# Kernel tuning notes

Measured on AMD Instinct MI355X. Metric: run time of the kernel, lower is better.

Reference implementation:

```python
import jax, jax.numpy as jnp
import numpy as np

DT = 0.1
EM_DX_DUMMY = 100.0  # dummy_value_set['em_delta_x']
EM_DV_DUMMY = 0.0    # dummy_value_set['em_delta_v']
ALPHA = 0.3          # keras LeakyReLU default
B, T, F = 32768, 50, 11
PROJ, U = 64, 128
MC = 3
IN_DIM = PROJ + U + 6 + MC  # 201


def setup_inputs() -> dict:
    key = jax.random.key(0)
    ks = jax.random.split(key, 16)
    def rn(k, shape, scale=0.05):
        return jax.random.normal(k, shape, dtype=jnp.float32) * scale
    return {
        'proj_latent': rn(ks[0], (B, PROJ), 1.0),
        'enc_h': rn(ks[1], (B, U), 1.0),
        'idm_s': jax.random.uniform(ks[2], (B, T, F), dtype=jnp.float32),
        'merger_cs': rn(ks[3], (B, T, MC), 1.0),
        'scaler_mean': rn(ks[4], (6,), 1.0),
        'scaler_var': jax.random.uniform(ks[5], (6,), dtype=jnp.float32) + 0.5,
        'W_lstm': rn(ks[6], (IN_DIM, 4 * U)),
        'U_lstm': rn(ks[7], (U, 4 * U)),
        'b_lstm': jnp.zeros((4 * U,), jnp.float32),
        'W1': rn(ks[8], (U, U)), 'b1': jnp.zeros((U,), jnp.float32),
        'W2': rn(ks[9], (U, U)), 'b2': jnp.zeros((U,), jnp.float32),
        'W3': rn(ks[10], (U, U)), 'b3': jnp.zeros((U,), jnp.float32),
        'Wa': rn(ks[11], (U, 1)), 'ba': jnp.zeros((1,), jnp.float32),
    }


def _lrelu(v):
    return jnp.where(v > 0, v, ALPHA * v)


def reference(proj_latent, enc_h, idm_s, merger_cs, scaler_mean, scaler_var,
              W_lstm, U_lstm, b_lstm, W1, b1, W2, b2, W3, b3, Wa, ba):
    b = idm_s.shape[0]
    u = W1.shape[0]
    inv_std = 1.0 / jnp.sqrt(scaler_var)

    def step(carry, xs):
        h, c, ego_v, ego_x, disp, prev_act = carry
        s, mc, t = xs  # s: [b,F], mc: [b,MC]
        first = (t == 0)
        f_veh_v = s[:, 1:2]
        m_veh_v = s[:, 2:3]
        f_glob_x = s[:, 4:5]
        m_glob_x = s[:, 5:6]
        m_exists = s[:, -1:]
        # physics update (skipped at step 0 where state is read from idm_s)
        new_v = jnp.where(first, s[:, 0:1], ego_v + prev_act * DT)
        delta = new_v * DT + 0.5 * prev_act * DT * DT
        new_x = jnp.where(first, s[:, 3:4], ego_x + delta)
        new_d = jnp.where(first, jnp.zeros_like(disp), disp + delta)
        ef_dx = f_glob_x - new_x
        em_dx = (m_glob_x - new_x) * m_exists + (1.0 - m_exists) * EM_DX_DUMMY
        ef_dv = new_v - f_veh_v
        em_dv = (new_v - m_veh_v) * m_exists + (1.0 - m_exists) * EM_DV_DUMMY
        env = jnp.concatenate([new_v, f_veh_v, ef_dv, ef_dx, em_dv, em_dx], axis=-1)
        env = (env - scaler_mean) * inv_std
        inp = jnp.concatenate([proj_latent, enc_h, env, mc], axis=-1)  # [b, 201]
        # keras LSTM cell: gate order i, f, g(candidate), o
        z = inp @ W_lstm + h @ U_lstm + b_lstm
        i = jax.nn.sigmoid(z[:, :u])
        f = jax.nn.sigmoid(z[:, u:2 * u])
        g = jnp.tanh(z[:, 2 * u:3 * u])
        o = jax.nn.sigmoid(z[:, 3 * u:])
        c2 = f * c + i * g
        h2 = o * jnp.tanh(c2)
        x1 = _lrelu(h2 @ W1 + b1)
        x2 = _lrelu(x1 @ W2 + b2)
        x3 = _lrelu(x2 @ W3 + b3)
        act = x3 @ Wa + ba  # [b, 1]
        return (h2, c2, new_v, new_x, new_d, act), (new_d, act)

    z1 = jnp.zeros((b, u), jnp.float32)
    one = jnp.zeros((b, 1), jnp.float32)
    carry0 = (z1, z1, one, one, one, one)
    xs = (jnp.swapaxes(idm_s, 0, 1), jnp.swapaxes(merger_cs, 0, 1),
          jnp.arange(idm_s.shape[1]))
    _, (disp_seq, act_seq) = jax.lax.scan(step, carry0, xs)
    # [T,b,1] -> [b,T,1]
    return jnp.swapaxes(disp_seq, 0, 1), jnp.swapaxes(act_seq, 0, 1)
```

## Files before the change

kernel.cpp:

```cpp
#include <hip/hip_runtime.h>

typedef unsigned short ushort_t;
typedef unsigned int uint_t;
typedef __bf16 v8bf __attribute__((ext_vector_type(8)));
typedef float v4f __attribute__((ext_vector_type(4)));

#define DTC 0.1f
#define NB 32768
#define NT 50

union U8 { v8bf v; ushort_t s[8]; };

__device__ __forceinline__ ushort_t f2bf(float f) {
  uint_t u = __float_as_uint(f);
  u += 0x7fffu + ((u >> 16) & 1u);
  return (ushort_t)(u >> 16);
}
__device__ __forceinline__ float bf2f(ushort_t s) {
  return __uint_as_float(((uint_t)s) << 16);
}
__device__ __forceinline__ float sigm(float x) {
  return __builtin_amdgcn_rcpf(1.f + __expf(-x));
}
__device__ __forceinline__ float tanhf_(float x) {
  return 1.f - 2.f * __builtin_amdgcn_rcpf(1.f + __expf(2.f * x));
}

__device__ __forceinline__ v8bf opaque(v8bf x) {
  union { v8bf v; uint_t u[4]; } t; t.v = x;
  asm volatile("" : "+v"(t.u[0]), "+v"(t.u[1]), "+v"(t.u[2]), "+v"(t.u[3]));
  return t.v;
}


__global__ __launch_bounds__(512) __attribute__((amdgpu_waves_per_eu(2, 2)))
void fsim_kernel(
    const float* __restrict__ proj, const float* __restrict__ ench,
    const float* __restrict__ idm,  const float* __restrict__ mcs,
    const float* __restrict__ smean,const float* __restrict__ svar,
    const float* __restrict__ Wl,   const float* __restrict__ Ul,
    const float* __restrict__ bl,   const float* __restrict__ W1,
    const float* __restrict__ b1,   const float* __restrict__ W2,
    const float* __restrict__ b2,   const float* __restrict__ W3,
    const float* __restrict__ b3,   const float* __restrict__ Wa,
    const float* __restrict__ ba,   float* __restrict__ out) {
  __shared__ __align__(16) short sh[81184];
  short* pe   = sh;
  short* h_s  = sh;
  short* xa_s = sh + 8704;
  short* xb_s = sh + 17408;
  short* ex_s = sh + 26112;
  float* sdf  = (float*)(sh + 28672);
  float* carr = (float*)(sh + 31232);
  float* wa_s = (float*)(sh + 31744);
  float* nrm  = (float*)(sh + 32000);
  float* part = (float*)(sh + 17408);
  short* w1_l = sh + 32032;
  short* w2_l = sh + 48416;
  short* w3_l = sh + 64800;

  const int tid  = threadIdx.x;
  const int wg   = blockIdx.x;
  const int w    = tid >> 6;
  const int l    = tid & 63;
  const int quad = l >> 4;
  const int c16  = l & 15;
  const int colz = w * 16 + c16;

  float* out_disp = out;
  float* out_act  = out + (size_t)NB * NT;

  const int eA = tid / 10, fA = tid - eA * 10;
  const float* pfpA; int pstA;
  if (fA < 7) { pfpA = idm + (size_t)(wg * 64 + eA) * 550 + ((fA == 6) ? 10 : fA); pstA = 11; }
  else        { pfpA = mcs + (size_t)(wg * 64 + eA) * 150 + (fA - 7);              pstA = 3;  }
  const int iB = tid + 512;
  const int eB = iB / 10, fB = iB - eB * 10;
  const float* pfpB; int pstB;
  if (fB < 7) { pfpB = idm + (size_t)(wg * 64 + eB) * 550 + ((fB == 6) ? 10 : fB); pstB = 11; }
  else        { pfpB = mcs + (size_t)(wg * 64 + eB) * 150 + (fB - 7);              pstB = 3;  }
  float pfA = pfpA[0];
  float pfB = (tid < 128) ? pfpB[0] : 0.f;

  v8bf Uf[4][4];
#pragma unroll
  for (int kc = 0; kc < 4; ++kc) {
#pragma unroll
    for (int g = 0; g < 4; ++g) {
      U8 u;
#pragma unroll
      for (int j = 0; j < 8; ++j)
        u.s[j] = f2bf(Ul[(kc * 32 + quad * 8 + j) * 512 + g * 128 + colz]);
      Uf[kc][g] = opaque(u.v);
    }
  }
  v8bf Ef[4];
#pragma unroll
  for (int g = 0; g < 4; ++g) {
    U8 u;
#pragma unroll
    for (int j = 0; j < 8; ++j) {
      int kk = quad * 8 + j;
      ushort_t val = 0;
      if (kk < 27) {
        int jj = kk % 9;
        float wv = Wl[(192 + jj) * 512 + g * 128 + colz];
        ushort_t hi = f2bf(wv);
        val = (kk < 9) ? hi : ((kk < 18) ? f2bf(wv - bf2f(hi)) : hi);
      }
      u.s[j] = val;
    }
    Ef[g] = opaque(u.v);
  }

#pragma unroll
  for (int kc = 0; kc < 4; ++kc) {
    U8 a, b, c;
#pragma unroll
    for (int j = 0; j < 8; ++j) {
      int row = kc * 32 + quad * 8 + j;
      a.s[j] = f2bf(W1[row * 128 + colz]);
      b.s[j] = f2bf(W2[row * 128 + colz]);
      c.s[j] = f2bf(W3[row * 128 + colz]);
    }
    *(v8bf*)(w1_l + (kc * 512 + tid) * 8) = a.v;
    *(v8bf*)(w2_l + (kc * 512 + tid) * 8) = b.v;
    *(v8bf*)(w3_l + (kc * 512 + tid) * 8) = c.v;
  }

  float bias1 = b1[colz], bias2 = b2[colz], bias3 = b3[colz];
  float ba_v  = ba[0];

  for (int i = tid; i < 2560; i += 512) ex_s[i] = 0;
  if (tid < 6) { nrm[tid] = smean[tid]; nrm[6 + tid] = 1.f / sqrtf(svar[tid]); }
  if (tid < 128) wa_s[tid] = Wa[tid];
  sdf[tid] = pfA;
  if (tid < 128) sdf[512 + tid] = pfB;

  for (int i = tid; i < 64 * 192; i += 512) {
    int e = i / 192, j = i - e * 192;
    float v = (j < 64) ? proj[(wg * 64 + e) * 64 + j]
                       : ench[(wg * 64 + e) * 128 + (j - 64)];
    pe[e * 200 + j] = (short)f2bf(v);
  }
  __syncthreads();

  uint_t base_pk[4][8];
#pragma unroll
  for (int mt = 0; mt < 4; ++mt) {
    v4f accz[4];
#pragma unroll
    for (int g = 0; g < 4; ++g) {
      float bz = bl[g * 128 + colz];
      accz[g] = (v4f){bz, bz, bz, bz};
    }
    for (int kc = 0; kc < 6; ++kc) {
      const v8bf a = *(const v8bf*)(pe + (mt * 16 + c16) * 200 + kc * 32 + quad * 8);
#pragma unroll
      for (int g = 0; g < 4; ++g) {
        U8 bu;
#pragma unroll
        for (int j = 0; j < 8; ++j)
          bu.s[j] = f2bf(Wl[(kc * 32 + quad * 8 + j) * 512 + g * 128 + colz]);
        accz[g] = __builtin_amdgcn_mfma_f32_16x16x32_bf16(a, bu.v, accz[g], 0, 0, 0);
      }
    }
#pragma unroll
    for (int g = 0; g < 4; ++g) {
      base_pk[mt][g * 2 + 0] = (uint_t)f2bf(accz[g][0]) | ((uint_t)f2bf(accz[g][1]) << 16);
      base_pk[mt][g * 2 + 1] = (uint_t)f2bf(accz[g][2]) | ((uint_t)f2bf(accz[g][3]) << 16);
    }
  }
  __syncthreads();

  for (int i = tid; i < 8704; i += 512) h_s[i] = 0;

  v4f c_st[4];
#pragma unroll
  for (int mt = 0; mt < 4; ++mt) c_st[mt] = (v4f){0.f, 0.f, 0.f, 0.f};

  for (int t = 0; t < NT; ++t) {
    if (t + 1 < NT) {
      pfA = pfpA[(size_t)(t + 1) * pstA];
      if (tid < 128) pfB = pfpB[(size_t)(t + 1) * pstB];
    }

    if (w == 0) {
      const int e  = l;
      const int ge = wg * 64 + e;
      const float* sp = sdf + (t & 1) * 640 + e * 10;
      float s0 = sp[0], s1 = sp[1], s2 = sp[2], s3 = sp[3];
      float s4 = sp[4], s5 = sp[5], s10 = sp[6];
      float mc0 = sp[7], mc1 = sp[8], mc2 = sp[9];
      float pa = 0.f, vv = 0.f, xx = 0.f, dd = 0.f;
      if (t != 0) { pa = carr[192 + e]; vv = carr[e]; xx = carr[64 + e]; dd = carr[128 + e]; }
      float new_v = (t == 0) ? s0 : vv + pa * DTC;
      float delta = new_v * DTC + 0.5f * pa * DTC * DTC;
      float new_x = (t == 0) ? s3 : xx + delta;
      float new_d = (t == 0) ? 0.f : dd + delta;
      float env[9];
      env[0] = new_v;
      env[1] = s1;
      env[2] = new_v - s1;
      env[3] = s4 - new_x;
      env[4] = (new_v - s2) * s10;
      env[5] = (s5 - new_x) * s10 + (1.f - s10) * 100.f;
#pragma unroll
      for (int j = 0; j < 6; ++j) env[j] = (env[j] - nrm[j]) * nrm[6 + j];
      env[6] = mc0; env[7] = mc1; env[8] = mc2;
#pragma unroll
      for (int j = 0; j < 9; ++j) {
        ushort_t hi = f2bf(env[j]);
        ushort_t lo = f2bf(env[j] - bf2f(hi));
        ex_s[e * 40 + j]      = (short)hi;
        ex_s[e * 40 + 9 + j]  = (short)hi;
        ex_s[e * 40 + 18 + j] = (short)lo;
      }
      carr[e] = new_v; carr[64 + e] = new_x; carr[128 + e] = new_d;
      out_disp[(size_t)ge * NT + t] = new_d;
    }
    __syncthreads();

    v4f h2v[4];
#pragma unroll
    for (int mt = 0; mt < 4; ++mt) {
      v4f acc[4];
#pragma unroll
      for (int g = 0; g < 4; ++g) {
        uint_t w0 = base_pk[mt][g * 2 + 0], w1 = base_pk[mt][g * 2 + 1];
        acc[g][0] = __uint_as_float(w0 << 16);
        acc[g][1] = __uint_as_float(w0 & 0xffff0000u);
        acc[g][2] = __uint_as_float(w1 << 16);
        acc[g][3] = __uint_as_float(w1 & 0xffff0000u);
      }
#pragma unroll
      for (int kc = 0; kc < 4; ++kc) {
        const v8bf a = *(const v8bf*)(h_s + (mt * 16 + c16) * 136 + kc * 32 + quad * 8);
#pragma unroll
        for (int g = 0; g < 4; ++g)
          acc[g] = __builtin_amdgcn_mfma_f32_16x16x32_bf16(a, Uf[kc][g], acc[g], 0, 0, 0);
      }
      {
        const v8bf ax = *(const v8bf*)(ex_s + (mt * 16 + c16) * 40 + quad * 8);
#pragma unroll
        for (int g = 0; g < 4; ++g)
          acc[g] = __builtin_amdgcn_mfma_f32_16x16x32_bf16(ax, Ef[g], acc[g], 0, 0, 0);
      }
      v4f cc = c_st[mt], h2;
#pragma unroll
      for (int r = 0; r < 4; ++r) {
        float ig = sigm(acc[0][r]);
        float fg = sigm(acc[1][r]);
        float gg = tanhf_(acc[2][r]);
        float og = sigm(acc[3][r]);
        float c2 = fg * cc[r] + ig * gg;
        cc[r] = c2;
        h2[r] = og * tanhf_(c2);
      }
      c_st[mt] = cc;
      h2v[mt]  = h2;
    }
    __syncthreads();
#pragma unroll
    for (int mt = 0; mt < 4; ++mt)
#pragma unroll
      for (int r = 0; r < 4; ++r)
        h_s[(mt * 16 + quad * 4 + r) * 136 + colz] = (short)f2bf(h2v[mt][r]);
    __syncthreads();

    auto mlp_layer = [&](const short* S, const short* WL, float bias, short* D) {
      v8bf Wf[4];
#pragma unroll
      for (int kc = 0; kc < 4; ++kc)
        Wf[kc] = *(const v8bf*)(WL + (kc * 512 + tid) * 8);
      v4f xs[4];
#pragma unroll
      for (int mt = 0; mt < 4; ++mt) {
        v4f acc = (v4f){bias, bias, bias, bias};
#pragma unroll
        for (int kc = 0; kc < 4; ++kc) {
          const v8bf a = *(const v8bf*)(S + (mt * 16 + c16) * 136 + kc * 32 + quad * 8);
          acc = __builtin_amdgcn_mfma_f32_16x16x32_bf16(a, Wf[kc], acc, 0, 0, 0);
        }
#pragma unroll
        for (int r = 0; r < 4; ++r) { float v = acc[r]; acc[r] = (v > 0.f) ? v : 0.3f * v; }
        xs[mt] = acc;
      }
#pragma unroll
      for (int mt = 0; mt < 4; ++mt)
#pragma unroll
        for (int r = 0; r < 4; ++r)
          D[(mt * 16 + quad * 4 + r) * 136 + colz] = (short)f2bf(xs[mt][r]);
    };
    mlp_layer(h_s, w1_l, bias1, xa_s);
    __syncthreads();
    mlp_layer(xa_s, w2_l, bias2, xb_s);
    __syncthreads();
    mlp_layer(xb_s, w3_l, bias3, xa_s);
    __syncthreads();

    {
      int e = tid >> 3, p = tid & 7;
      float s = 0.f;
#pragma unroll
      for (int i = 0; i < 16; ++i) {
        int u = p * 16 + i;
        s += bf2f((ushort_t)xa_s[e * 136 + u]) * wa_s[u];
      }
      part[e * 8 + p] = s;
    }
    if (t + 1 < NT) {
      sdf[((t + 1) & 1) * 640 + tid] = pfA;
      if (tid < 128) sdf[((t + 1) & 1) * 640 + 512 + tid] = pfB;
    }
    __syncthreads();
    if (tid < 64) {
      float a = ba_v;
#pragma unroll
      for (int p = 0; p < 8; ++p) a += part[tid * 8 + p];
      carr[192 + tid] = a;
      out_act[(size_t)(wg * 64 + tid) * NT + t] = a;
    }
  }
}

extern "C" void kernel_launch(void* const* d_in, const int* in_sizes, int n_in,
                              void* d_out, int out_size, void* d_ws, size_t ws_size,
                              hipStream_t stream) {
  (void)in_sizes; (void)n_in; (void)out_size; (void)d_ws; (void)ws_size;
  fsim_kernel<<<dim3(512), dim3(512), 0, stream>>>(
      (const float*)d_in[0],  (const float*)d_in[1],  (const float*)d_in[2],
      (const float*)d_in[3],  (const float*)d_in[4],  (const float*)d_in[5],
      (const float*)d_in[6],  (const float*)d_in[7],  (const float*)d_in[8],
      (const float*)d_in[9],  (const float*)d_in[10], (const float*)d_in[11],
      (const float*)d_in[12], (const float*)d_in[13], (const float*)d_in[14],
      (const float*)d_in[15], (const float*)d_in[16], (float*)d_out);
}
```

Baseline: 967.2 us.

## Prepack weights to bf16 in a separate kernel and stream them from global memory

Adds a small pre-kernel that converts and packs the LSTM recurrent, env and MLP weights into MFMA fragment layout in the workspace each call. The main kernel stops holding U/E fragments in registers and stops staging MLP weights in LDS, instead reading them from global memory (expected to hit L1/L2) inside every time step. This frees registers and cuts LDS from about 162KB to 64KB, and the waves-per-EU hint rises from 2 to 4 to raise occupancy. The cost is many repeated global loads per step on the critical recurrent path, plus an extra launch.

New measurement: 2.834 ms. 2.93x slower.

```diff
diff --git a/kernel.cpp b/kernel.cpp
--- a/kernel.cpp
+++ b/kernel.cpp
@@ -26,25 +26,59 @@
   return 1.f - 2.f * __builtin_amdgcn_rcpf(1.f + __expf(2.f * x));
 }
 
-__device__ __forceinline__ v8bf opaque(v8bf x) {
-  union { v8bf v; uint_t u[4]; } t; t.v = x;
-  asm volatile("" : "+v"(t.u[0]), "+v"(t.u[1]), "+v"(t.u[2]), "+v"(t.u[3]));
-  return t.v;
-}
-
-
-__global__ __launch_bounds__(512) __attribute__((amdgpu_waves_per_eu(2, 2)))
+
+__global__ __launch_bounds__(512)
+void pack_kernel(const float* __restrict__ Ul, const float* __restrict__ Wl,
+                 const float* __restrict__ W1, const float* __restrict__ W2,
+                 const float* __restrict__ W3, ushort_t* __restrict__ ws) {
+  const int tid  = threadIdx.x;
+  const int b    = blockIdx.x;
+  const int l    = tid & 63;
+  const int wv   = tid >> 6;
+  const int quad = l >> 4;
+  const int c16  = l & 15;
+  const int colz = wv * 16 + c16;
+  U8 u;
+  if (b < 16) {
+    int kc = b >> 2, g = b & 3;
+#pragma unroll
+    for (int j = 0; j < 8; ++j)
+      u.s[j] = f2bf(Ul[(kc * 32 + quad * 8 + j) * 512 + g * 128 + colz]);
+  } else if (b < 20) {
+    int g = b - 16;
+#pragma unroll
+    for (int j = 0; j < 8; ++j) {
+      int kk = quad * 8 + j;
+      ushort_t val = 0;
+      if (kk < 27) {
+        int jj = kk % 9;
+        float wvv = Wl[(192 + jj) * 512 + g * 128 + colz];
+        ushort_t hi = f2bf(wvv);
+        val = (kk < 9) ? hi : ((kk < 18) ? f2bf(wvv - bf2f(hi)) : hi);
+      }
+      u.s[j] = val;
+    }
+  } else {
+    int m = (b - 20) >> 2, kc = (b - 20) & 3;
+    const float* Wp = (m == 0) ? W1 : ((m == 1) ? W2 : W3);
+#pragma unroll
+    for (int j = 0; j < 8; ++j)
+      u.s[j] = f2bf(Wp[(kc * 32 + quad * 8 + j) * 128 + colz]);
+  }
+  *(v8bf*)(ws + (size_t)b * 4096 + (size_t)tid * 8) = u.v;
+}
+
+__global__ __launch_bounds__(512) __attribute__((amdgpu_waves_per_eu(4, 4)))
 void fsim_kernel(
     const float* __restrict__ proj, const float* __restrict__ ench,
     const float* __restrict__ idm,  const float* __restrict__ mcs,
     const float* __restrict__ smean,const float* __restrict__ svar,
-    const float* __restrict__ Wl,   const float* __restrict__ Ul,
-    const float* __restrict__ bl,   const float* __restrict__ W1,
-    const float* __restrict__ b1,   const float* __restrict__ W2,
-    const float* __restrict__ b2,   const float* __restrict__ W3,
+    const float* __restrict__ Wl,   const float* __restrict__ bl,
+    const float* __restrict__ b1,   const float* __restrict__ b2,
     const float* __restrict__ b3,   const float* __restrict__ Wa,
-    const float* __restrict__ ba,   float* __restrict__ out) {
-  __shared__ __align__(16) short sh[81184];
+    const float* __restrict__ ba,   const ushort_t* __restrict__ ws,
+    float* __restrict__ out) {
+  __shared__ __align__(16) short sh[32032];
   short* pe   = sh;
   short* h_s  = sh;
   short* xa_s = sh + 8704;
@@ -55,9 +89,6 @@
   float* wa_s = (float*)(sh + 31744);
   float* nrm  = (float*)(sh + 32000);
   float* part = (float*)(sh + 17408);
-  short* w1_l = sh + 32032;
-  short* w2_l = sh + 48416;
-  short* w3_l = sh + 64800;
 
   const int tid  = threadIdx.x;
   const int wg   = blockIdx.x;
@@ -69,6 +100,7 @@
 
   float* out_disp = out;
   float* out_act  = out + (size_t)NB * NT;
+  const ushort_t* wsb = ws + (size_t)tid * 8;
 
   const int eA = tid / 10, fA = tid - eA * 10;
   const float* pfpA; int pstA;
@@ -81,52 +113,6 @@
   else        { pfpB = mcs + (size_t)(wg * 64 + eB) * 150 + (fB - 7);              pstB = 3;  }
   float pfA = pfpA[0];
   float pfB = (tid < 128) ? pfpB[0] : 0.f;
-
-  v8bf Uf[4][4];
-#pragma unroll
-  for (int kc = 0; kc < 4; ++kc) {
-#pragma unroll
-    for (int g = 0; g < 4; ++g) {
-      U8 u;
-#pragma unroll
-      for (int j = 0; j < 8; ++j)
-        u.s[j] = f2bf(Ul[(kc * 32 + quad * 8 + j) * 512 + g * 128 + colz]);
-      Uf[kc][g] = opaque(u.v);
-    }
-  }
-  v8bf Ef[4];
-#pragma unroll
-  for (int g = 0; g < 4; ++g) {
-    U8 u;
-#pragma unroll
-    for (int j = 0; j < 8; ++j) {
-      int kk = quad * 8 + j;
-      ushort_t val = 0;
-      if (kk < 27) {
-        int jj = kk % 9;
-        float wv = Wl[(192 + jj) * 512 + g * 128 + colz];
-        ushort_t hi = f2bf(wv);
-        val = (kk < 9) ? hi : ((kk < 18) ? f2bf(wv - bf2f(hi)) : hi);
-      }
-      u.s[j] = val;
-    }
-    Ef[g] = opaque(u.v);
-  }
-
-#pragma unroll
-  for (int kc = 0; kc < 4; ++kc) {
-    U8 a, b, c;
-#pragma unroll
-    for (int j = 0; j < 8; ++j) {
-      int row = kc * 32 + quad * 8 + j;
-      a.s[j] = f2bf(W1[row * 128 + colz]);
-      b.s[j] = f2bf(W2[row * 128 + colz]);
-      c.s[j] = f2bf(W3[row * 128 + colz]);
-    }
-    *(v8bf*)(w1_l + (kc * 512 + tid) * 8) = a.v;
-    *(v8bf*)(w2_l + (kc * 512 + tid) * 8) = b.v;
-    *(v8bf*)(w3_l + (kc * 512 + tid) * 8) = c.v;
-  }
 
   float bias1 = b1[colz], bias2 = b2[colz], bias3 = b3[colz];
   float ba_v  = ba[0];
@@ -237,14 +223,18 @@
       for (int kc = 0; kc < 4; ++kc) {
         const v8bf a = *(const v8bf*)(h_s + (mt * 16 + c16) * 136 + kc * 32 + quad * 8);
 #pragma unroll
-        for (int g = 0; g < 4; ++g)
-          acc[g] = __builtin_amdgcn_mfma_f32_16x16x32_bf16(a, Uf[kc][g], acc[g], 0, 0, 0);
+        for (int g = 0; g < 4; ++g) {
+          const v8bf uf = *(const v8bf*)(wsb + (size_t)(kc * 4 + g) * 4096);
+          acc[g] = __builtin_amdgcn_mfma_f32_16x16x32_bf16(a, uf, acc[g], 0, 0, 0);
+        }
       }
       {
         const v8bf ax = *(const v8bf*)(ex_s + (mt * 16 + c16) * 40 + quad * 8);
 #pragma unroll
-        for (int g = 0; g < 4; ++g)
-          acc[g] = __builtin_amdgcn_mfma_f32_16x16x32_bf16(ax, Ef[g], acc[g], 0, 0, 0);
+        for (int g = 0; g < 4; ++g) {
+          const v8bf ef = *(const v8bf*)(wsb + (size_t)(16 + g) * 4096);
+          acc[g] = __builtin_amdgcn_mfma_f32_16x16x32_bf16(ax, ef, acc[g], 0, 0, 0);
+        }
       }
       v4f cc = c_st[mt], h2;
 #pragma unroll
@@ -268,11 +258,11 @@
         h_s[(mt * 16 + quad * 4 + r) * 136 + colz] = (short)f2bf(h2v[mt][r]);
     __syncthreads();
 
-    auto mlp_layer = [&](const short* S, const short* WL, float bias, short* D) {
+    auto mlp_layer = [&](const short* S, const ushort_t* WF, float bias, short* D) {
       v8bf Wf[4];
 #pragma unroll
       for (int kc = 0; kc < 4; ++kc)
-        Wf[kc] = *(const v8bf*)(WL + (kc * 512 + tid) * 8);
+        Wf[kc] = *(const v8bf*)(WF + (size_t)kc * 4096);
       v4f xs[4];
 #pragma unroll
       for (int mt = 0; mt < 4; ++mt) {
@@ -292,11 +282,11 @@
         for (int r = 0; r < 4; ++r)
           D[(mt * 16 + quad * 4 + r) * 136 + colz] = (short)f2bf(xs[mt][r]);
     };
-    mlp_layer(h_s, w1_l, bias1, xa_s);
-    __syncthreads();
-    mlp_layer(xa_s, w2_l, bias2, xb_s);
-    __syncthreads();
-    mlp_layer(xb_s, w3_l, bias3, xa_s);
+    mlp_layer(h_s, wsb + (size_t)20 * 4096, bias1, xa_s);
+    __syncthreads();
+    mlp_layer(xa_s, wsb + (size_t)24 * 4096, bias2, xb_s);
+    __syncthreads();
+    mlp_layer(xb_s, wsb + (size_t)28 * 4096, bias3, xa_s);
     __syncthreads();
 
     {
@@ -327,12 +317,14 @@
 extern "C" void kernel_launch(void* const* d_in, const int* in_sizes, int n_in,
                               void* d_out, int out_size, void* d_ws, size_t ws_size,
                               hipStream_t stream) {
-  (void)in_sizes; (void)n_in; (void)out_size; (void)d_ws; (void)ws_size;
+  (void)in_sizes; (void)n_in; (void)out_size; (void)ws_size;
+  pack_kernel<<<dim3(32), dim3(512), 0, stream>>>(
+      (const float*)d_in[7],  (const float*)d_in[6],  (const float*)d_in[9],
+      (const float*)d_in[11], (const float*)d_in[13], (ushort_t*)d_ws);
   fsim_kernel<<<dim3(512), dim3(512), 0, stream>>>(
       (const float*)d_in[0],  (const float*)d_in[1],  (const float*)d_in[2],
       (const float*)d_in[3],  (const float*)d_in[4],  (const float*)d_in[5],
-      (const float*)d_in[6],  (const float*)d_in[7],  (const float*)d_in[8],
-      (const float*)d_in[9],  (const float*)d_in[10], (const float*)d_in[11],
-      (const float*)d_in[12], (const float*)d_in[13], (const float*)d_in[14],
-      (const float*)d_in[15], (const float*)d_in[16], (float*)d_out);
-}
+      (const float*)d_in[6],  (const float*)d_in[8],  (const float*)d_in[10],
+      (const float*)d_in[12], (const float*)d_in[14], (const float*)d_in[15],
+      (const float*)d_in[16], (const ushort_t*)d_ws,  (float*)d_out);
+}
```

## Double-buffer LSTM hidden state, keep MLP weights in registers, shuffle-reduce the action head

Applied to the files above, without the earlier changes.

Ping-pongs the hidden-state LDS buffer so the new h is written right after the gate math, with no extra barrier. The MLP weights now live in registers, and three quarters of the recurrent U matrix moves to LDS to free VGPRs. The output projection is reduced with lane shuffles, and the environment update is spread across all waves. Together these remove several __syncthreads per timestep and LDS round-trips, at the cost of extra LDS reads of U every step and higher register pressure.

Result: slower. 1.017 ms (+5.2%).

```diff
diff --git a/kernel.cpp b/kernel.cpp
--- a/kernel.cpp
+++ b/kernel.cpp
@@ -46,18 +46,15 @@
     const float* __restrict__ ba,   float* __restrict__ out) {
   __shared__ __align__(16) short sh[81184];
   short* pe   = sh;
-  short* h_s  = sh;
-  short* xa_s = sh + 8704;
-  short* xb_s = sh + 17408;
+  short* hA   = sh;
+  short* hB   = sh + 8704;
+  short* xa_s = sh + 17408;
   short* ex_s = sh + 26112;
   float* sdf  = (float*)(sh + 28672);
   float* carr = (float*)(sh + 31232);
   float* wa_s = (float*)(sh + 31744);
   float* nrm  = (float*)(sh + 32000);
-  float* part = (float*)(sh + 17408);
-  short* w1_l = sh + 32032;
-  short* w2_l = sh + 48416;
-  short* w3_l = sh + 64800;
+  short* u_lds= sh + 32032;
 
   const int tid  = threadIdx.x;
   const int wg   = blockIdx.x;
@@ -82,17 +79,25 @@
   float pfA = pfpA[0];
   float pfB = (tid < 128) ? pfpB[0] : 0.f;
 
-  v8bf Uf[4][4];
-#pragma unroll
-  for (int kc = 0; kc < 4; ++kc) {
+#pragma unroll
+  for (int kc = 0; kc < 3; ++kc) {
 #pragma unroll
     for (int g = 0; g < 4; ++g) {
       U8 u;
 #pragma unroll
       for (int j = 0; j < 8; ++j)
         u.s[j] = f2bf(Ul[(kc * 32 + quad * 8 + j) * 512 + g * 128 + colz]);
-      Uf[kc][g] = opaque(u.v);
-    }
+      *(v8bf*)(u_lds + ((kc * 4 + g) * 512 + tid) * 8) = u.v;
+    }
+  }
+  v8bf Uf3[4];
+#pragma unroll
+  for (int g = 0; g < 4; ++g) {
+    U8 u;
+#pragma unroll
+    for (int j = 0; j < 8; ++j)
+      u.s[j] = f2bf(Ul[(96 + quad * 8 + j) * 512 + g * 128 + colz]);
+    Uf3[g] = opaque(u.v);
   }
   v8bf Ef[4];
 #pragma unroll
@@ -112,7 +117,7 @@
     }
     Ef[g] = opaque(u.v);
   }
-
+  v8bf W1f[4], W2f[4], W3f[4];
 #pragma unroll
   for (int kc = 0; kc < 4; ++kc) {
     U8 a, b, c;
@@ -123,11 +128,8 @@
       b.s[j] = f2bf(W2[row * 128 + colz]);
       c.s[j] = f2bf(W3[row * 128 + colz]);
     }
-    *(v8bf*)(w1_l + (kc * 512 + tid) * 8) = a.v;
-    *(v8bf*)(w2_l + (kc * 512 + tid) * 8) = b.v;
-    *(v8bf*)(w3_l + (kc * 512 + tid) * 8) = c.v;
-  }
-
+    W1f[kc] = opaque(a.v); W2f[kc] = opaque(b.v); W3f[kc] = opaque(c.v);
+  }
   float bias1 = b1[colz], bias2 = b2[colz], bias3 = b3[colz];
   float ba_v  = ba[0];
 
@@ -173,20 +175,23 @@
   }
   __syncthreads();
 
-  for (int i = tid; i < 8704; i += 512) h_s[i] = 0;
+  for (int i = tid; i < 8704; i += 512) hA[i] = 0;
 
   v4f c_st[4];
 #pragma unroll
   for (int mt = 0; mt < 4; ++mt) c_st[mt] = (v4f){0.f, 0.f, 0.f, 0.f};
 
   for (int t = 0; t < NT; ++t) {
+    short* rd = (t & 1) ? hB : hA;
+    short* wr = (t & 1) ? hA : hB;
+
     if (t + 1 < NT) {
       pfA = pfpA[(size_t)(t + 1) * pstA];
       if (tid < 128) pfB = pfpB[(size_t)(t + 1) * pstB];
     }
 
-    if (w == 0) {
-      const int e  = l;
+    if ((l & 7) == 0) {
+      const int e  = w * 8 + (l >> 3);
       const int ge = wg * 64 + e;
       const float* sp = sdf + (t & 1) * 640 + e * 10;
       float s0 = sp[0], s1 = sp[1], s2 = sp[2], s3 = sp[3];
@@ -221,58 +226,66 @@
     }
     __syncthreads();
 
-    v4f h2v[4];
-#pragma unroll
-    for (int mt = 0; mt < 4; ++mt) {
-      v4f acc[4];
-#pragma unroll
-      for (int g = 0; g < 4; ++g) {
-        uint_t w0 = base_pk[mt][g * 2 + 0], w1 = base_pk[mt][g * 2 + 1];
-        acc[g][0] = __uint_as_float(w0 << 16);
-        acc[g][1] = __uint_as_float(w0 & 0xffff0000u);
-        acc[g][2] = __uint_as_float(w1 << 16);
-        acc[g][3] = __uint_as_float(w1 & 0xffff0000u);
+#pragma unroll
+    for (int half = 0; half < 2; ++half) {
+      v4f acc[2][4];
+#pragma unroll
+      for (int m2 = 0; m2 < 2; ++m2) {
+        int mt = half * 2 + m2;
+#pragma unroll
+        for (int g = 0; g < 4; ++g) {
+          uint_t w0 = base_pk[mt][g * 2 + 0], w1 = base_pk[mt][g * 2 + 1];
+          acc[m2][g][0] = __uint_as_float(w0 << 16);
+          acc[m2][g][1] = __uint_as_float(w0 & 0xffff0000u);
+          acc[m2][g][2] = __uint_as_float(w1 << 16);
+          acc[m2][g][3] = __uint_as_float(w1 & 0xffff0000u);
+        }
+      }
+      {
+        const v8bf ax0 = *(const v8bf*)(ex_s + ((half * 2 + 0) * 16 + c16) * 40 + quad * 8);
+        const v8bf ax1 = *(const v8bf*)(ex_s + ((half * 2 + 1) * 16 + c16) * 40 + quad * 8);
+#pragma unroll
+        for (int g = 0; g < 4; ++g) {
+          acc[0][g] = __builtin_amdgcn_mfma_f32_16x16x32_bf16(ax0, Ef[g], acc[0][g], 0, 0, 0);
+          acc[1][g] = __builtin_amdgcn_mfma_f32_16x16x32_bf16(ax1, Ef[g], acc[1][g], 0, 0, 0);
+        }
       }
 #pragma unroll
       for (int kc = 0; kc < 4; ++kc) {
-        const v8bf a = *(const v8bf*)(h_s + (mt * 16 + c16) * 136 + kc * 32 + quad * 8);
-#pragma unroll
-        for (int g = 0; g < 4; ++g)
-          acc[g] = __builtin_amdgcn_mfma_f32_16x16x32_bf16(a, Uf[kc][g], acc[g], 0, 0, 0);
-      }
-      {
-        const v8bf ax = *(const v8bf*)(ex_s + (mt * 16 + c16) * 40 + quad * 8);
-#pragma unroll
-        for (int g = 0; g < 4; ++g)
-          acc[g] = __builtin_amdgcn_mfma_f32_16x16x32_bf16(ax, Ef[g], acc[g], 0, 0, 0);
-      }
-      v4f cc = c_st[mt], h2;
-#pragma unroll
-      for (int r = 0; r < 4; ++r) {
-        float ig = sigm(acc[0][r]);
-        float fg = sigm(acc[1][r]);
-        float gg = tanhf_(acc[2][r]);
-        float og = sigm(acc[3][r]);
-        float c2 = fg * cc[r] + ig * gg;
-        cc[r] = c2;
-        h2[r] = og * tanhf_(c2);
-      }
-      c_st[mt] = cc;
-      h2v[mt]  = h2;
-    }
-    __syncthreads();
-#pragma unroll
-    for (int mt = 0; mt < 4; ++mt)
-#pragma unroll
-      for (int r = 0; r < 4; ++r)
-        h_s[(mt * 16 + quad * 4 + r) * 136 + colz] = (short)f2bf(h2v[mt][r]);
-    __syncthreads();
-
-    auto mlp_layer = [&](const short* S, const short* WL, float bias, short* D) {
-      v8bf Wf[4];
-#pragma unroll
-      for (int kc = 0; kc < 4; ++kc)
-        Wf[kc] = *(const v8bf*)(WL + (kc * 512 + tid) * 8);
+        const v8bf a0 = *(const v8bf*)(rd + ((half * 2 + 0) * 16 + c16) * 136 + kc * 32 + quad * 8);
+        const v8bf a1 = *(const v8bf*)(rd + ((half * 2 + 1) * 16 + c16) * 136 + kc * 32 + quad * 8);
+#pragma unroll
+        for (int g = 0; g < 4; ++g) {
+          v8bf uf;
+          if (kc < 3) uf = *(const v8bf*)(u_lds + ((kc * 4 + g) * 512 + tid) * 8);
+          else        uf = Uf3[g];
+          acc[0][g] = __builtin_amdgcn_mfma_f32_16x16x32_bf16(a0, uf, acc[0][g], 0, 0, 0);
+          acc[1][g] = __builtin_amdgcn_mfma_f32_16x16x32_bf16(a1, uf, acc[1][g], 0, 0, 0);
+        }
+      }
+#pragma unroll
+      for (int m2 = 0; m2 < 2; ++m2) {
+        int mt = half * 2 + m2;
+        v4f cc = c_st[mt], h2;
+#pragma unroll
+        for (int r = 0; r < 4; ++r) {
+          float ig = sigm(acc[m2][0][r]);
+          float fg = sigm(acc[m2][1][r]);
+          float gg = tanhf_(acc[m2][2][r]);
+          float og = sigm(acc[m2][3][r]);
+          float c2 = fg * cc[r] + ig * gg;
+          cc[r] = c2;
+          h2[r] = og * tanhf_(c2);
+        }
+        c_st[mt] = cc;
+#pragma unroll
+        for (int r = 0; r < 4; ++r)
+          wr[(mt * 16 + quad * 4 + r) * 136 + colz] = (short)f2bf(h2[r]);
+      }
+    }
+    __syncthreads();
+
+    auto mlp_layer = [&](const short* S, const v8bf* Wf, float bias, short* D) {
       v4f xs[4];
 #pragma unroll
       for (int mt = 0; mt < 4; ++mt) {
@@ -292,34 +305,34 @@
         for (int r = 0; r < 4; ++r)
           D[(mt * 16 + quad * 4 + r) * 136 + colz] = (short)f2bf(xs[mt][r]);
     };
-    mlp_layer(h_s, w1_l, bias1, xa_s);
-    __syncthreads();
-    mlp_layer(xa_s, w2_l, bias2, xb_s);
-    __syncthreads();
-    mlp_layer(xb_s, w3_l, bias3, xa_s);
-    __syncthreads();
-
-    {
-      int e = tid >> 3, p = tid & 7;
-      float s = 0.f;
-#pragma unroll
-      for (int i = 0; i < 16; ++i) {
-        int u = p * 16 + i;
-        s += bf2f((ushort_t)xa_s[e * 136 + u]) * wa_s[u];
-      }
-      part[e * 8 + p] = s;
-    }
+    mlp_layer(wr,   W1f, bias1, xa_s);
+    __syncthreads();
+    mlp_layer(xa_s, W2f, bias2, rd);
+    __syncthreads();
+    mlp_layer(rd,   W3f, bias3, xa_s);
     if (t + 1 < NT) {
       sdf[((t + 1) & 1) * 640 + tid] = pfA;
       if (tid < 128) sdf[((t + 1) & 1) * 640 + 512 + tid] = pfB;
     }
     __syncthreads();
-    if (tid < 64) {
-      float a = ba_v;
-#pragma unroll
-      for (int p = 0; p < 8; ++p) a += part[tid * 8 + p];
-      carr[192 + tid] = a;
-      out_act[(size_t)(wg * 64 + tid) * NT + t] = a;
+
+    {
+      const int r = w * 8 + (l >> 3);
+      const int p = l & 7;
+      float s = 0.f;
+#pragma unroll
+      for (int i = 0; i < 16; ++i) {
+        int u = p * 16 + i;
+        s += bf2f((ushort_t)xa_s[r * 136 + u]) * wa_s[u];
+      }
+      s += __shfl_xor(s, 1);
+      s += __shfl_xor(s, 2);
+      s += __shfl_xor(s, 4);
+      if ((l & 7) == 0) {
+        float a = s + ba_v;
+        carr[192 + r] = a;
+        out_act[(size_t)(wg * 64 + r) * NT + t] = a;
+      }
     }
   }
 }
```
